# Kernel optimization log

Hardware: AMD Instinct MI355X
Metric: run time of the kernel (lower is better)

The kernel has to match this reference:

```python
import jax, jax.numpy as jnp
import numpy as np

EPS = 1e-6
NUM_ITERS = 8
TEMPERATURE = 1.0


def setup_inputs() -> dict:
    key = jax.random.key(0)
    k1, k2 = jax.random.split(key)
    x = jax.random.normal(k1, (4, 8192, 4096), dtype=jnp.float32)
    # nn.Linear(dim, num_experts, bias=False) weight: [num_experts, dim]
    w_gate = jax.random.normal(k2, (64, 4096), dtype=jnp.float32) * (1.0 / np.sqrt(4096))
    return {"x": x, "w_gate": w_gate}


def sinkhorn(t, num_iters=NUM_ITERS, temperature=TEMPERATURE, eps=EPS):
    # t: [b, n, e] raw gate logits (pre-log)
    t = jnp.log(jnp.clip(t, eps))  # log(clamp(t, min=eps))
    t = t / temperature
    for _ in range(num_iters):
        t = t - jax.nn.logsumexp(t, axis=-2, keepdims=True)  # normalize over tokens
        t = t - jax.nn.logsumexp(t, axis=-1, keepdims=True)  # normalize over experts
    return jnp.exp(t)


def reference(x, w_gate):
    # gate projection: [b, n, d] @ [e, d]^T -> [b, n, e]
    gates = jnp.einsum('bnd,ed->bne', x, w_gate)
    return sinkhorn(gates)
```

## Files before the change

### kernel.cpp

```cpp
#include <hip/hip_runtime.h>
#include <hip/hip_bf16.h>
#include <hip/hip_fp16.h>

#define B_ 4
#define N_ 8192
#define D_ 4096
#define E_ 64
#define M_ (B_ * N_)
#define BM 64
#define BK 64
#define NK (D_ / BK)

typedef _Float16 half8 __attribute__((ext_vector_type(8)));
typedef float f32x4 __attribute__((ext_vector_type(4)));

__global__ __launch_bounds__(512, 4) void gemm_log(const float* __restrict__ x,
                                                   const float* __restrict__ w,
                                                   float* __restrict__ t0,
                                                   float* __restrict__ S1) {
  __shared__ _Float16 As[2][BM * BK];
  __shared__ _Float16 Bs[2][E_ * BK];
  __shared__ float wsum[8][32];

  const int tid = threadIdx.x;
  const int lane = tid & 63;
  const int wv = tid >> 6;
  const int wm = (wv >> 1) * 16;
  const int wn = (wv & 1) * 32;
  const int l15 = lane & 15;
  const int lq = lane >> 4;
  const int rowBase = blockIdx.x * BM;
  const int b = rowBase / N_;

  const int sr = tid >> 3;
  const int su = tid & 7;
  const size_t xoff = (size_t)(rowBase + sr) * D_ + su * 8;
  const size_t woff = (size_t)sr * D_ + su * 8;
  const int sdst = sr * 64 + ((su ^ (sr & 7)) << 3);

  const int arow = wm + l15;
  int aoff[2], boff[2][2];
#pragma unroll
  for (int ks = 0; ks < 2; ++ks)
    aoff[ks] = arow * 64 + (((ks * 4 + lq) ^ (arow & 7)) << 3);
#pragma unroll
  for (int ni = 0; ni < 2; ++ni) {
    const int bcol = wn + ni * 16 + l15;
#pragma unroll
    for (int ks = 0; ks < 2; ++ks)
      boff[ni][ks] = bcol * 64 + (((ks * 4 + lq) ^ (bcol & 7)) << 3);
  }

  f32x4 acc[2] = {};
  float4 xa, xb, wa, wb;

  xa = *(const float4*)&x[xoff];     xb = *(const float4*)&x[xoff + 4];
  wa = *(const float4*)&w[woff];     wb = *(const float4*)&w[woff + 4];

  for (int kc = 0; kc < NK; ++kc) {
    const int cur = kc & 1;
    half8 hx, hw;
    hx[0] = (_Float16)xa.x; hx[1] = (_Float16)xa.y; hx[2] = (_Float16)xa.z; hx[3] = (_Float16)xa.w;
    hx[4] = (_Float16)xb.x; hx[5] = (_Float16)xb.y; hx[6] = (_Float16)xb.z; hx[7] = (_Float16)xb.w;
    hw[0] = (_Float16)wa.x; hw[1] = (_Float16)wa.y; hw[2] = (_Float16)wa.z; hw[3] = (_Float16)wa.w;
    hw[4] = (_Float16)wb.x; hw[5] = (_Float16)wb.y; hw[6] = (_Float16)wb.z; hw[7] = (_Float16)wb.w;
    *(half8*)&As[cur][sdst] = hx;
    *(half8*)&Bs[cur][sdst] = hw;

    if (kc + 1 < NK) {
      const size_t o = (size_t)(kc + 1) * BK;
      xa = *(const float4*)&x[xoff + o]; xb = *(const float4*)&x[xoff + o + 4];
      wa = *(const float4*)&w[woff + o]; wb = *(const float4*)&w[woff + o + 4];
    }

    asm volatile("s_waitcnt lgkmcnt(0)" ::: "memory");
    __builtin_amdgcn_s_barrier();

    half8 a0 = *(const half8*)&As[cur][aoff[0]];
    half8 a1 = *(const half8*)&As[cur][aoff[1]];
    half8 b00 = *(const half8*)&Bs[cur][boff[0][0]];
    half8 b01 = *(const half8*)&Bs[cur][boff[0][1]];
    half8 b10 = *(const half8*)&Bs[cur][boff[1][0]];
    half8 b11 = *(const half8*)&Bs[cur][boff[1][1]];
    acc[0] = __builtin_amdgcn_mfma_f32_16x16x32_f16(a0, b00, acc[0], 0, 0, 0);
    acc[0] = __builtin_amdgcn_mfma_f32_16x16x32_f16(a1, b01, acc[0], 0, 0, 0);
    acc[1] = __builtin_amdgcn_mfma_f32_16x16x32_f16(a0, b10, acc[1], 0, 0, 0);
    acc[1] = __builtin_amdgcn_mfma_f32_16x16x32_f16(a1, b11, acc[1], 0, 0, 0);
  }

  float lsum[2] = {0.f, 0.f};
#pragma unroll
  for (int ni = 0; ni < 2; ++ni) {
#pragma unroll
    for (int r = 0; r < 4; ++r) {
      const float v = fmaxf(acc[ni][r], 1e-6f);
      const int grow = rowBase + wm + lq * 4 + r;
      const int gcol = wn + ni * 16 + l15;
      t0[(size_t)grow * E_ + gcol] = __logf(v);
      lsum[ni] += v;
    }
  }
#pragma unroll
  for (int ni = 0; ni < 2; ++ni) {
    float v = lsum[ni];
    v += __shfl_xor(v, 16);
    v += __shfl_xor(v, 32);
    if (lq == 0) wsum[wv][ni * 16 + l15] = v;
  }
  __syncthreads();
  if (tid < 64) {
    const int e = tid;
    const int half = e >> 5;
    const int idx = e & 31;
    const float tot = wsum[0 * 2 + half][idx] + wsum[1 * 2 + half][idx] +
                      wsum[2 * 2 + half][idx] + wsum[3 * 2 + half][idx];
    atomicAdd(&S1[b * E_ + e], tot);
  }
}

__global__ __launch_bounds__(256) void sinkhorn_iter(const float* __restrict__ t0,
                                                     float* __restrict__ slots,
                                                     float* __restrict__ out,
                                                     int it, int last) {
  const int tid = threadIdx.x;
  const int lane = tid & 63;
  const int wv = tid >> 6;
  const int b = blockIdx.x >> 8;
  const int chunk = blockIdx.x & 255;

  float C = __logf(slots[b * E_ + lane]);
  for (int j = 1; j < it; ++j) C += __logf(slots[j * (B_ * E_) + b * E_ + lane]);

  float colacc = 0.f;
  const int nbase = chunk * 32 + wv * 8;
#pragma unroll
  for (int i = 0; i < 8; ++i) {
    const int n = nbase + i;
    const float v = t0[((size_t)b * N_ + n) * E_ + lane];
    const float p = __expf(v - C);
    float s = p;
    s += __shfl_xor(s, 1);  s += __shfl_xor(s, 2);  s += __shfl_xor(s, 4);
    s += __shfl_xor(s, 8);  s += __shfl_xor(s, 16); s += __shfl_xor(s, 32);
    const float q = p / s;
    if (last) out[((size_t)b * N_ + n) * E_ + lane] = q;
    else      colacc += q;
  }
  if (!last) {
    __shared__ float wsum[4][64];
    wsum[wv][lane] = colacc;
    __syncthreads();
    if (tid < 64) {
      const float tot = wsum[0][tid] + wsum[1][tid] + wsum[2][tid] + wsum[3][tid];
      atomicAdd(&slots[it * (B_ * E_) + b * E_ + tid], tot);
    }
  }
}

extern "C" void kernel_launch(void* const* d_in, const int* in_sizes, int n_in,
                              void* d_out, int out_size, void* d_ws, size_t ws_size,
                              hipStream_t stream) {
  (void)in_sizes; (void)n_in; (void)out_size; (void)ws_size;
  const float* x = (const float*)d_in[0];
  const float* w = (const float*)d_in[1];
  float* out = (float*)d_out;
  float* slots = (float*)d_ws;

  hipMemsetAsync(slots, 0, 8 * B_ * E_ * sizeof(float), stream);
  gemm_log<<<M_ / BM, 512, 0, stream>>>(x, w, out, slots);
  for (int it = 1; it <= 8; ++it)
    sinkhorn_iter<<<B_ * 256, 256, 0, stream>>>(out, slots, out, it, it == 8 ? 1 : 0);
}
```

Baseline: 218.4 us.

## Drop LDS staging in gate GEMM; load fragments directly from global with pre-converted fp16 weights

```diff
diff --git a/kernel.cpp b/kernel.cpp
--- a/kernel.cpp
+++ b/kernel.cpp
@@ -1,5 +1,4 @@
 #include <hip/hip_runtime.h>
-#include <hip/hip_bf16.h>
 #include <hip/hip_fp16.h>
 
 #define B_ 4
@@ -7,114 +6,104 @@
 #define D_ 4096
 #define E_ 64
 #define M_ (B_ * N_)
-#define BM 64
-#define BK 64
-#define NK (D_ / BK)
+#define NK 64
 
 typedef _Float16 half8 __attribute__((ext_vector_type(8)));
 typedef float f32x4 __attribute__((ext_vector_type(4)));
 
-__global__ __launch_bounds__(512, 4) void gemm_log(const float* __restrict__ x,
-                                                   const float* __restrict__ w,
+union H4 { _Float16 h[4]; uint2 u2; };
+
+__global__ __launch_bounds__(256) void convert_w(const float* __restrict__ w,
+                                                 _Float16* __restrict__ w16) {
+  const int i = (blockIdx.x * 256 + threadIdx.x) * 4;
+  const float4 v = *(const float4*)&w[i];
+  H4 h;
+  h.h[0] = (_Float16)v.x; h.h[1] = (_Float16)v.y;
+  h.h[2] = (_Float16)v.z; h.h[3] = (_Float16)v.w;
+  *(uint2*)&w16[i] = h.u2;
+}
+
+__global__ __launch_bounds__(256, 2) void gemm_log(const float* __restrict__ x,
+                                                   const _Float16* __restrict__ w16,
                                                    float* __restrict__ t0,
-                                                   float* __restrict__ S1) {
-  __shared__ _Float16 As[2][BM * BK];
-  __shared__ _Float16 Bs[2][E_ * BK];
-  __shared__ float wsum[8][32];
-
+                                                   float* __restrict__ slot0) {
   const int tid = threadIdx.x;
   const int lane = tid & 63;
   const int wv = tid >> 6;
-  const int wm = (wv >> 1) * 16;
-  const int wn = (wv & 1) * 32;
   const int l15 = lane & 15;
   const int lq = lane >> 4;
-  const int rowBase = blockIdx.x * BM;
-  const int b = rowBase / N_;
+  const int row16 = (blockIdx.x * 4 + wv) * 16;
+  const int b = row16 >> 13;
 
-  const int sr = tid >> 3;
-  const int su = tid & 7;
-  const size_t xoff = (size_t)(rowBase + sr) * D_ + su * 8;
-  const size_t woff = (size_t)sr * D_ + su * 8;
-  const int sdst = sr * 64 + ((su ^ (sr & 7)) << 3);
+  const float* xA = x + (size_t)(row16 + l15) * D_ + lq * 8;
+  const _Float16* wB = w16 + (size_t)l15 * D_ + lq * 8;
 
-  const int arow = wm + l15;
-  int aoff[2], boff[2][2];
+  f32x4 acc[4] = {};
+
+  struct Regs {
+    float4 a0, a1, a2, a3;
+    half8 bfr[8];
+  };
+  Regs rA, rB;
+
+#define LOADC(R, KC)                                                        \
+  do {                                                                      \
+    const int o_ = (KC) * 64;                                               \
+    (R).a0 = *(const float4*)(xA + o_);                                     \
+    (R).a1 = *(const float4*)(xA + o_ + 4);                                 \
+    (R).a2 = *(const float4*)(xA + o_ + 32);                                \
+    (R).a3 = *(const float4*)(xA + o_ + 36);                                \
+    _Pragma("unroll")                                                       \
+    for (int ni = 0; ni < 4; ++ni) {                                        \
+      (R).bfr[ni * 2 + 0] = *(const half8*)(wB + (size_t)ni * 16 * D_ + o_);      \
+      (R).bfr[ni * 2 + 1] = *(const half8*)(wB + (size_t)ni * 16 * D_ + o_ + 32); \
+    }                                                                       \
+  } while (0)
+
+#define COMPC(R)                                                            \
+  do {                                                                      \
+    half8 af0, af1;                                                         \
+    af0[0] = (_Float16)(R).a0.x; af0[1] = (_Float16)(R).a0.y;               \
+    af0[2] = (_Float16)(R).a0.z; af0[3] = (_Float16)(R).a0.w;               \
+    af0[4] = (_Float16)(R).a1.x; af0[5] = (_Float16)(R).a1.y;               \
+    af0[6] = (_Float16)(R).a1.z; af0[7] = (_Float16)(R).a1.w;               \
+    af1[0] = (_Float16)(R).a2.x; af1[1] = (_Float16)(R).a2.y;               \
+    af1[2] = (_Float16)(R).a2.z; af1[3] = (_Float16)(R).a2.w;               \
+    af1[4] = (_Float16)(R).a3.x; af1[5] = (_Float16)(R).a3.y;               \
+    af1[6] = (_Float16)(R).a3.z; af1[7] = (_Float16)(R).a3.w;               \
+    _Pragma("unroll")                                                       \
+    for (int ni = 0; ni < 4; ++ni) {                                        \
+      acc[ni] = __builtin_amdgcn_mfma_f32_16x16x32_f16(af0, (R).bfr[ni * 2 + 0], acc[ni], 0, 0, 0); \
+      acc[ni] = __builtin_amdgcn_mfma_f32_16x16x32_f16(af1, (R).bfr[ni * 2 + 1], acc[ni], 0, 0, 0); \
+    }                                                                       \
+  } while (0)
+
+  LOADC(rA, 0);
+  for (int kc = 0; kc < NK; kc += 2) {
+    LOADC(rB, kc + 1);
+    COMPC(rA);
+    if (kc + 2 < NK) LOADC(rA, kc + 2);
+    COMPC(rB);
+  }
+#undef LOADC
+#undef COMPC
+
+  float lsum[4];
 #pragma unroll
-  for (int ks = 0; ks < 2; ++ks)
-    aoff[ks] = arow * 64 + (((ks * 4 + lq) ^ (arow & 7)) << 3);
-#pragma unroll
-  for (int ni = 0; ni < 2; ++ni) {
-    const int bcol = wn + ni * 16 + l15;
-#pragma unroll
-    for (int ks = 0; ks < 2; ++ks)
-      boff[ni][ks] = bcol * 64 + (((ks * 4 + lq) ^ (bcol & 7)) << 3);
-  }
-
-  f32x4 acc[2] = {};
-  float4 xa, xb, wa, wb;
-
-  xa = *(const float4*)&x[xoff];     xb = *(const float4*)&x[xoff + 4];
-  wa = *(const float4*)&w[woff];     wb = *(const float4*)&w[woff + 4];
-
-  for (int kc = 0; kc < NK; ++kc) {
-    const int cur = kc & 1;
-    half8 hx, hw;
-    hx[0] = (_Float16)xa.x; hx[1] = (_Float16)xa.y; hx[2] = (_Float16)xa.z; hx[3] = (_Float16)xa.w;
-    hx[4] = (_Float16)xb.x; hx[5] = (_Float16)xb.y; hx[6] = (_Float16)xb.z; hx[7] = (_Float16)xb.w;
-    hw[0] = (_Float16)wa.x; hw[1] = (_Float16)wa.y; hw[2] = (_Float16)wa.z; hw[3] = (_Float16)wa.w;
-    hw[4] = (_Float16)wb.x; hw[5] = (_Float16)wb.y; hw[6] = (_Float16)wb.z; hw[7] = (_Float16)wb.w;
-    *(half8*)&As[cur][sdst] = hx;
-    *(half8*)&Bs[cur][sdst] = hw;
-
-    if (kc + 1 < NK) {
-      const size_t o = (size_t)(kc + 1) * BK;
-      xa = *(const float4*)&x[xoff + o]; xb = *(const float4*)&x[xoff + o + 4];
-      wa = *(const float4*)&w[woff + o]; wb = *(const float4*)&w[woff + o + 4];
-    }
-
-    asm volatile("s_waitcnt lgkmcnt(0)" ::: "memory");
-    __builtin_amdgcn_s_barrier();
-
-    half8 a0 = *(const half8*)&As[cur][aoff[0]];
-    half8 a1 = *(const half8*)&As[cur][aoff[1]];
-    half8 b00 = *(const half8*)&Bs[cur][boff[0][0]];
-    half8 b01 = *(const half8*)&Bs[cur][boff[0][1]];
-    half8 b10 = *(const half8*)&Bs[cur][boff[1][0]];
-    half8 b11 = *(const half8*)&Bs[cur][boff[1][1]];
-    acc[0] = __builtin_amdgcn_mfma_f32_16x16x32_f16(a0, b00, acc[0], 0, 0, 0);
-    acc[0] = __builtin_amdgcn_mfma_f32_16x16x32_f16(a1, b01, acc[0], 0, 0, 0);
-    acc[1] = __builtin_amdgcn_mfma_f32_16x16x32_f16(a0, b10, acc[1], 0, 0, 0);
-    acc[1] = __builtin_amdgcn_mfma_f32_16x16x32_f16(a1, b11, acc[1], 0, 0, 0);
-  }
-
-  float lsum[2] = {0.f, 0.f};
-#pragma unroll
-  for (int ni = 0; ni < 2; ++ni) {
+  for (int ni = 0; ni < 4; ++ni) {
+    lsum[ni] = 0.f;
 #pragma unroll
     for (int r = 0; r < 4; ++r) {
       const float v = fmaxf(acc[ni][r], 1e-6f);
-      const int grow = rowBase + wm + lq * 4 + r;
-      const int gcol = wn + ni * 16 + l15;
+      const int grow = row16 + lq * 4 + r;
+      const int gcol = ni * 16 + l15;
       t0[(size_t)grow * E_ + gcol] = __logf(v);
       lsum[ni] += v;
     }
-  }
-#pragma unroll
-  for (int ni = 0; ni < 2; ++ni) {
     float v = lsum[ni];
     v += __shfl_xor(v, 16);
     v += __shfl_xor(v, 32);
-    if (lq == 0) wsum[wv][ni * 16 + l15] = v;
-  }
-  __syncthreads();
-  if (tid < 64) {
-    const int e = tid;
-    const int half = e >> 5;
-    const int idx = e & 31;
-    const float tot = wsum[0 * 2 + half][idx] + wsum[1 * 2 + half][idx] +
-                      wsum[2 * 2 + half][idx] + wsum[3 * 2 + half][idx];
-    atomicAdd(&S1[b * E_ + e], tot);
+    if (lq == 0) atomicAdd(&slot0[b * E_ + ni * 16 + l15], v);
   }
 }
 
@@ -164,9 +153,11 @@
   const float* w = (const float*)d_in[1];
   float* out = (float*)d_out;
   float* slots = (float*)d_ws;
+  _Float16* w16 = (_Float16*)((char*)d_ws + 8192);
 
   hipMemsetAsync(slots, 0, 8 * B_ * E_ * sizeof(float), stream);
-  gemm_log<<<M_ / BM, 512, 0, stream>>>(x, w, out, slots);
+  convert_w<<<(E_ * D_) / 1024, 256, 0, stream>>>(w, w16);
+  gemm_log<<<M_ / 64, 256, 0, stream>>>(x, w16, out, slots);
   for (int it = 1; it <= 8; ++it)
     sinkhorn_iter<<<B_ * 256, 256, 0, stream>>>(out, slots, out, it, it == 8 ? 1 : 0);
 }
```

Result: slower. 284.4 us (+30.2%).
